# Optimization experiments

Measured on AMD Instinct MI355X. Metric: run time of the kernel, lower is better.

The kernel has to match this reference:

```python
import jax, jax.numpy as jnp
import numpy as np

SPATIAL, CROP = 128, 256


def definePsf(N, M, slope):
    # standard LCT psf (O'Toole et al.), as used in Wenzheng Chen's torch port
    x = (np.arange(2 * N, dtype=np.float32) / (2 * N - 1)) * 2 - 1
    z = (np.arange(2 * M, dtype=np.float32) / (2 * M - 1)) * 2
    gy, gx = np.meshgrid(x, x)
    psf = np.abs(((4 * slope) ** 2) * (gx[None] ** 2 + gy[None] ** 2) - z[:, None, None])
    psf = (psf == psf.min(axis=0, keepdims=True)).astype(np.float32)
    psf = psf / psf[:, N, N].sum()
    psf = psf / np.linalg.norm(psf.ravel())
    psf = np.roll(psf, N, axis=1)
    psf = np.roll(psf, N, axis=2)
    return psf


def resamplingOperator(M):
    row = M ** 2
    x = np.arange(row, dtype=np.float64) + 1
    mtx = np.zeros((row, M), dtype=np.float64)
    mtx[np.arange(row), (np.ceil(np.sqrt(x)) - 1).astype(np.int64)] = 1
    mtx = mtx / x[:, None]
    mtxi = mtx.T.copy()
    for _ in range(int(np.log2(M))):
        mtx = 0.5 * (mtx[0::2] + mtx[1::2])
        mtxi = 0.5 * (mtxi[:, 0::2] + mtxi[:, 1::2])
    return mtx.astype(np.float32), mtxi.astype(np.float32)


def setup_inputs() -> dict:
    key = jax.random.key(0)
    k1, k2 = jax.random.split(key)
    B, D, T, H = 1, 1, CROP, SPATIAL
    feture = jax.random.uniform(k1, (B, D, T, H, H), dtype=jnp.float32)

    c = 3e8
    bin_len = 0.01
    wall_size = 2.0
    trange = CROP * c * (bin_len / c)
    slope = (wall_size / 2.0) / trange
    psf = definePsf(SPATIAL, CROP, slope)
    fpsf = np.fft.fftn(psf)
    snr = 0.1
    invpsf = np.conjugate(fpsf) / (1.0 / snr + np.real(fpsf) ** 2 + np.imag(fpsf) ** 2)

    mtx, mtxi = resamplingOperator(CROP)
    gridz = (np.arange(CROP, dtype=np.float32) / (CROP - 1)).reshape(1, CROP, 1, 1)
    learnable_w = 0.01 * jax.random.normal(k2, (2,) + psf.shape, dtype=jnp.float32)

    return dict(
        feture=feture,
        gridz=jnp.asarray(gridz),
        mtx=jnp.asarray(mtx),
        mtxi=jnp.asarray(mtxi),
        invpsf_real=jnp.asarray(np.real(invpsf).astype(np.float32)),
        invpsf_imag=jnp.asarray(np.imag(invpsf).astype(np.float32)),
        learnable_w=learnable_w,
    )


def reference(feture, gridz, mtx, mtxi, invpsf_real, invpsf_imag, learnable_w):
    B, D, T, H, W = feture.shape
    # diffuse falloff compensation: * z^4
    data = feture.reshape(B * D, T, H, W) * gridz ** 4
    # temporal resampling GEMM: [M,T] @ [BD,T,HW]
    tmp = jnp.einsum('mt,bthw->bmhw', mtx, data)
    # zero-pad to 2T x 2H x 2W
    pad = jnp.zeros((B * D, 2 * T, 2 * H, 2 * W), jnp.float32).at[:, :T, :H, :W].set(tmp)
    # full (non-onesided) complex 3D FFT of real data
    fre = jnp.fft.fftn(pad, axes=(1, 2, 3))
    # learned + fixed inverse filter in frequency domain
    wf = (learnable_w[0] + invpsf_real) + 1j * (learnable_w[1] + invpsf_imag)
    vol = jnp.fft.ifftn(fre * wf, axes=(1, 2, 3)).real[:, :T, :H, :W]
    # inverse temporal resampling GEMM
    out = jnp.einsum('mt,bthw->bmhw', mtxi, vol)
    return out.reshape(B, D, T, H, W)
```

## Files before the change

### kernel.cpp

```cpp
#include <hip/hip_runtime.h>
#include <math.h>

#define TC 256
#define HC 128
#define Z2 512
#define Y2 256
#define X2 256
#define HW 16384
#define LSTR256 260
#define LSTR512 519
#define MTSH 4
#define MT (1<<MTSH)
#define WPAD 132
#define KZS 257

__device__ __forceinline__ float2 cadd(float2 a, float2 b){ return make_float2(a.x+b.x, a.y+b.y); }
__device__ __forceinline__ float2 csub(float2 a, float2 b){ return make_float2(a.x-b.x, a.y-b.y); }

template<int SGN>
__device__ __forceinline__ float2 cmul_tw(float2 z, float2 w){
  float wy = (SGN < 0) ? w.y : -w.y;
  return make_float2(z.x*w.x - z.y*wy, z.x*wy + z.y*w.x);
}
template<int SGN>
__device__ __forceinline__ float2 mul_pmi(float2 t){
  return (SGN < 0) ? make_float2(t.y, -t.x) : make_float2(-t.y, t.x);
}

template<int SGN>
__device__ __forceinline__ void dft16(float2 r[16], const float2* __restrict__ tw){
  float2 u[16];
  #pragma unroll
  for (int b2=0;b2<4;b2++){
    float2 x0=r[b2], x1=r[4+b2], x2=r[8+b2], x3=r[12+b2];
    float2 t0=cadd(x0,x2), t1=csub(x0,x2), t2=cadd(x1,x3), t3=csub(x1,x3);
    float2 y0=cadd(t0,t2), y2=csub(t0,t2);
    float2 t3i = mul_pmi<SGN>(t3);
    float2 y1=cadd(t1,t3i), y3=csub(t1,t3i);
    u[0*4+b2]=y0;
    u[1*4+b2]=cmul_tw<SGN>(y1, tw[(16*b2)&255]);
    u[2*4+b2]=cmul_tw<SGN>(y2, tw[(32*b2)&255]);
    u[3*4+b2]=cmul_tw<SGN>(y3, tw[(48*b2)&255]);
  }
  #pragma unroll
  for (int e2=0;e2<4;e2++){
    float2 x0=u[e2*4+0], x1=u[e2*4+1], x2=u[e2*4+2], x3=u[e2*4+3];
    float2 t0=cadd(x0,x2), t1=csub(x0,x2), t2=cadd(x1,x3), t3=csub(x1,x3);
    float2 t3i = mul_pmi<SGN>(t3);
    r[0*4+e2]=cadd(t0,t2);
    r[1*4+e2]=cadd(t1,t3i);
    r[2*4+e2]=csub(t0,t2);
    r[3*4+e2]=csub(t1,t3i);
  }
}

template<int SGN>
__device__ __forceinline__ void fft256(float2* ln, int b, const float2* __restrict__ tw){
  float2 r[16];
  #pragma unroll
  for (int a=0;a<16;a++) r[a] = ln[16*a+b];
  dft16<SGN>(r, tw);
  #pragma unroll
  for (int e=1;e<16;e++) r[e] = cmul_tw<SGN>(r[e], tw[(b*e)&255]);
  __syncthreads();
  #pragma unroll
  for (int e=0;e<16;e++) ln[16*e+b] = r[e];
  __syncthreads();
  #pragma unroll
  for (int a=0;a<16;a++) r[a] = ln[16*b+a];
  dft16<SGN>(r, tw);
  __syncthreads();
  #pragma unroll
  for (int d=0;d<16;d++) ln[16*d+b] = r[d];
  __syncthreads();
}

template<int SGN, bool CROP_OUT>
__device__ __forceinline__ void fft512(float2* ln, int lt,
        const float2* __restrict__ tw256, const float2* __restrict__ tw512){
  int team = lt >> 4, b = lt & 15;
  float2* sc = ln + team*256;
  float2 r[16];
  #pragma unroll
  for (int a=0;a<16;a++) r[a] = ln[2*(16*a+b) + team];
  dft16<SGN>(r, tw256);
  #pragma unroll
  for (int e=1;e<16;e++) r[e] = cmul_tw<SGN>(r[e], tw256[(b*e)&255]);
  __syncthreads();
  #pragma unroll
  for (int e=0;e<16;e++) sc[16*e+b] = r[e];
  __syncthreads();
  #pragma unroll
  for (int a=0;a<16;a++) r[a] = sc[16*b+a];
  dft16<SGN>(r, tw256);
  __syncthreads();
  if (team==0){
    #pragma unroll
    for (int d=0;d<16;d++) ln[16*d+b] = r[d];
  } else {
    #pragma unroll
    for (int d=0;d<16;d++){ int k=16*d+b; ln[256+k] = cmul_tw<SGN>(r[d], tw512[k]); }
  }
  __syncthreads();
  float2 res[8], res2[8];
  #pragma unroll
  for (int j=0;j<8;j++){
    int k = lt + 32*j;
    float2 E = ln[k], WO = ln[256+k];
    res[j]  = cadd(E,WO);
    res2[j] = csub(E,WO);
  }
  __syncthreads();
  #pragma unroll
  for (int j=0;j<8;j++){
    int k = lt + 32*j;
    ln[k] = res[j];
    if (!CROP_OUT) ln[256+k] = res2[j];
  }
  __syncthreads();
}

__global__ void k_init_tw(float2* tw256, float2* tw512){
  int j = threadIdx.x;
  if (j < 512){
    double a = -6.283185307179586476925286766559 * (double)j / 512.0;
    tw512[j] = make_float2((float)cos(a), (float)sin(a));
  }
  if (j < 256){
    double a = -6.283185307179586476925286766559 * (double)j / 256.0;
    tw256[j] = make_float2((float)cos(a), (float)sin(a));
  }
}

__global__ __launch_bounds__(256) void k_gemm(const float* __restrict__ A,
    const float* __restrict__ Bv, const float* __restrict__ gz, float* __restrict__ C){
  __shared__ float As[64][MT];
  __shared__ float zz[256];
  int tid = threadIdx.x;
  int hw0 = blockIdx.x*512 + tid*2;
  int m0 = blockIdx.y*MT;
  float2 acc[MT];
  #pragma unroll
  for (int i=0;i<MT;i++) acc[i]=make_float2(0.f,0.f);
  {
    float s = 1.f;
    if (gz){ float g = gz[tid]; float g2=g*g; s = g2*g2; }
    zz[tid] = s;
  }
  for (int t0=0;t0<256;t0+=64){
    __syncthreads();
    #pragma unroll
    for (int e=0;e<(64*MT)/256;e++){
      int idx = e*256 + tid;
      int tt = idx >> MTSH, mi = idx & (MT-1);
      As[tt][mi] = A[(size_t)(m0+mi)*256 + t0 + tt] * zz[t0+tt];
    }
    __syncthreads();
    for (int ts=0;ts<64;ts+=8){
      float2 v[8];
      #pragma unroll
      for (int j=0;j<8;j++) v[j] = *(const float2*)(Bv + (size_t)(t0+ts+j)*HW + hw0);
      #pragma unroll
      for (int j=0;j<8;j++){
        const float4* row = (const float4*)&As[ts+j][0];
        #pragma unroll
        for (int q=0;q<MT/4;q++){
          float4 a4 = row[q];
          acc[4*q+0].x += a4.x*v[j].x; acc[4*q+0].y += a4.x*v[j].y;
          acc[4*q+1].x += a4.y*v[j].x; acc[4*q+1].y += a4.y*v[j].y;
          acc[4*q+2].x += a4.z*v[j].x; acc[4*q+2].y += a4.z*v[j].y;
          acc[4*q+3].x += a4.w*v[j].x; acc[4*q+3].y += a4.w*v[j].y;
        }
      }
    }
  }
  #pragma unroll
  for (int mi=0;mi<MT;mi++) *(float2*)(C + (size_t)(m0+mi)*HW + hw0) = acc[mi];
}

__global__ __launch_bounds__(256) void k_fft_zf(const float* __restrict__ tmp,
      float2* __restrict__ A, const float2* __restrict__ tw256, const float2* __restrict__ tw512){
  __shared__ float2 buf[8*LSTR512];
  int tid = threadIdx.x;
  int w = tid & 7, lt = tid >> 3;
  int hw = blockIdx.x*8 + w;
  int h = hw >> 7, wx = hw & 127;
  float2* ln = buf + w*LSTR512;
  #pragma unroll
  for (int a=0;a<16;a++){
    int n = 32*a + lt;
    ln[n] = (n<256) ? make_float2(tmp[(size_t)n*HW + hw], 0.f) : make_float2(0.f,0.f);
  }
  __syncthreads();
  fft512<-1,false>(ln, lt, tw256, tw512);
  size_t colbase = (size_t)h*WPAD + wx;
  #pragma unroll
  for (int a=0;a<8;a++){
    int n = 32*a + lt;
    A[(size_t)n*(128*WPAD) + colbase] = ln[n];
  }
  if (lt==0) A[(size_t)256*(128*WPAD) + colbase] = ln[256];
}

__global__ __launch_bounds__(256) void k_fft_yf(const float2* __restrict__ A,
      float2* __restrict__ B, const float2* __restrict__ tw256){
  __shared__ float2 buf[16*LSTR256];
  int tid = threadIdx.x;
  int w = tid & 15, b = tid >> 4;
  int kz = blockIdx.x;
  int wx = blockIdx.y*16 + w;
  float2* ln = buf + w*LSTR256;
  size_t abase = (size_t)kz*(128*WPAD) + wx;
  #pragma unroll
  for (int a=0;a<8;a++){
    int n = 16*a + b;
    ln[n] = A[abase + (size_t)n*WPAD];
    ln[n+128] = make_float2(0.f,0.f);
  }
  __syncthreads();
  fft256<-1>(ln, b, tw256);
  size_t bbase = (size_t)kz*(256*WPAD) + wx;
  #pragma unroll
  for (int a=0;a<16;a++){
    int n = 16*a + b;
    B[bbase + (size_t)n*WPAD] = ln[n];
  }
}

__global__ __launch_bounds__(256) void k_x_filt(float2* __restrict__ B,
      const float* __restrict__ R, const float* __restrict__ I,
      const float* __restrict__ w0, const float* __restrict__ w1,
      const float2* __restrict__ tw256){
  __shared__ float2 buf[16*LSTR256];
  const float sc = 1.f/33554432.f;
  int tid = threadIdx.x;
  int wl = tid >> 4, b = tid & 15;
  int kz = blockIdx.y;
  int ky = blockIdx.x*16 + wl;
  float2* ln = buf + wl*LSTR256;
  size_t rb = ((size_t)kz*256 + ky)*WPAD;
  #pragma unroll
  for (int a=0;a<8;a++){
    int n = 16*a + b;
    ln[n] = B[rb + n];
    ln[n+128] = make_float2(0.f,0.f);
  }
  __syncthreads();
  fft256<-1>(ln, b, tw256);
  unsigned mz = (512u - (unsigned)kz) & 511u;
  unsigned my = (256u - (unsigned)ky) & 255u;
  size_t trow = ((size_t)kz<<16) + (size_t)ky*256;
  size_t mrow = ((size_t)mz<<16) + (size_t)my*256;
  #pragma unroll
  for (int a=0;a<16;a++){
    int kx = 16*a + b;
    int mx = (256 - kx) & 255;
    float wr = (R[trow+kx] + 0.5f*(w0[trow+kx] + w0[mrow+mx]))*sc;
    float wi = (I[trow+kx] + 0.5f*(w1[trow+kx] - w1[mrow+mx]))*sc;
    float2 v = ln[kx];
    ln[kx] = make_float2(v.x*wr - v.y*wi, v.x*wi + v.y*wr);
  }
  fft256<1>(ln, b, tw256);
  #pragma unroll
  for (int a=0;a<8;a++){
    int n = 16*a + b;
    B[rb + n] = ln[n];
  }
}

__global__ __launch_bounds__(256) void k_fft_yi(const float2* __restrict__ B,
      float2* __restrict__ A, const float2* __restrict__ tw256){
  __shared__ float2 buf[16*LSTR256];
  int tid = threadIdx.x;
  int w = tid & 15, b = tid >> 4;
  int kz = blockIdx.x;
  int wx = blockIdx.y*16 + w;
  float2* ln = buf + w*LSTR256;
  size_t bbase = (size_t)kz*(256*WPAD) + wx;
  #pragma unroll
  for (int a=0;a<16;a++){
    int n = 16*a + b;
    ln[n] = B[bbase + (size_t)n*WPAD];
  }
  __syncthreads();
  fft256<1>(ln, b, tw256);
  size_t abase = (size_t)kz*(128*WPAD) + wx;
  #pragma unroll
  for (int a=0;a<8;a++){
    int n = 16*a + b;
    A[abase + (size_t)n*WPAD] = ln[n];
  }
}

__global__ __launch_bounds__(256) void k_fft_zi(const float2* __restrict__ A,
      float* __restrict__ vol, const float2* __restrict__ tw256, const float2* __restrict__ tw512){
  __shared__ float2 buf[8*LSTR512];
  int tid = threadIdx.x;
  int w = tid & 7, lt = tid >> 3;
  int hw = blockIdx.x*8 + w;
  int h = hw >> 7, wx = hw & 127;
  float2* ln = buf + w*LSTR512;
  size_t colbase = (size_t)h*WPAD + wx;
  #pragma unroll
  for (int a=0;a<8;a++){
    int n = 32*a + lt;
    ln[n] = A[(size_t)n*(128*WPAD) + colbase];
  }
  if (lt==0) ln[256] = A[(size_t)256*(128*WPAD) + colbase];
  __syncthreads();
  #pragma unroll
  for (int a=8;a<16;a++){
    int n = 32*a + lt;
    if (n > 256){ float2 v = ln[512-n]; ln[n] = make_float2(v.x, -v.y); }
  }
  __syncthreads();
  fft512<1,true>(ln, lt, tw256, tw512);
  #pragma unroll
  for (int a=0;a<8;a++){
    int n = 32*a + lt;
    vol[(size_t)n*HW + hw] = ln[n].x;
  }
}

extern "C" void kernel_launch(void* const* d_in, const int* in_sizes, int n_in,
                              void* d_out, int out_size, void* d_ws, size_t ws_size,
                              hipStream_t stream) {
  const float* fet = (const float*)d_in[0];
  const float* gz  = (const float*)d_in[1];
  const float* mtx = (const float*)d_in[2];
  const float* mtxi= (const float*)d_in[3];
  const float* Rr  = (const float*)d_in[4];
  const float* Ii  = (const float*)d_in[5];
  const float* lw  = (const float*)d_in[6];
  const float* w0  = lw;
  const float* w1  = lw + (size_t)Z2*Y2*X2;
  float* out = (float*)d_out;

  char* ws = (char*)d_ws;
  const size_t OFF_TW256 = 0;
  const size_t OFF_TW512 = 2048;
  const size_t OFF_TMP   = 8192;
  const size_t TMP_BYTES = (size_t)TC*HW*sizeof(float);
  const size_t OFF_A     = OFF_TMP + TMP_BYTES;
  const size_t A_BYTES   = (size_t)KZS*128*WPAD*sizeof(float2);
  const size_t OFF_B     = OFF_A + A_BYTES;
  const size_t B_BYTES   = (size_t)KZS*256*WPAD*sizeof(float2);
  const size_t NEED      = OFF_B + B_BYTES;
  if (ws_size < NEED) return;

  float2* tw256 = (float2*)(ws + OFF_TW256);
  float2* tw512 = (float2*)(ws + OFF_TW512);
  float*  tmp   = (float*)(ws + OFF_TMP);
  float*  vol   = (float*)(ws + OFF_TMP);
  float2* A     = (float2*)(ws + OFF_A);
  float2* B     = (float2*)(ws + OFF_B);

  hipLaunchKernelGGL(k_init_tw, dim3(1), dim3(512), 0, stream, tw256, tw512);
  hipLaunchKernelGGL(k_gemm, dim3(32,256/MT), dim3(256), 0, stream, mtx, fet, gz, tmp);
  hipLaunchKernelGGL(k_fft_zf, dim3(2048), dim3(256), 0, stream, tmp, A, tw256, tw512);
  hipLaunchKernelGGL(k_fft_yf, dim3(KZS,8), dim3(256), 0, stream, A, B, tw256);
  hipLaunchKernelGGL(k_x_filt, dim3(16,KZS), dim3(256), 0, stream, B, Rr, Ii, w0, w1, tw256);
  hipLaunchKernelGGL(k_fft_yi, dim3(KZS,8), dim3(256), 0, stream, B, A, tw256);
  hipLaunchKernelGGL(k_fft_zi, dim3(2048), dim3(256), 0, stream, A, vol, tw256, tw512);
  hipLaunchKernelGGL(k_gemm, dim3(32,256/MT), dim3(256), 0, stream, mtxi, vol, (const float*)nullptr, out);
}
```

Baseline: 308.3 us.

## Fuse y-forward, x-filter and y-inverse FFTs into one per-plane kernel

After: 421.2 us. 1.37x slower.

```diff
diff --git a/kernel.cpp b/kernel.cpp
--- a/kernel.cpp
+++ b/kernel.cpp
@@ -202,93 +202,105 @@
   if (lt==0) A[(size_t)256*(128*WPAD) + colbase] = ln[256];
 }
 
-__global__ __launch_bounds__(256) void k_fft_yf(const float2* __restrict__ A,
-      float2* __restrict__ B, const float2* __restrict__ tw256){
-  __shared__ float2 buf[16*LSTR256];
-  int tid = threadIdx.x;
-  int w = tid & 15, b = tid >> 4;
-  int kz = blockIdx.x;
-  int wx = blockIdx.y*16 + w;
-  float2* ln = buf + w*LSTR256;
-  size_t abase = (size_t)kz*(128*WPAD) + wx;
-  #pragma unroll
-  for (int a=0;a<8;a++){
-    int n = 16*a + b;
-    ln[n] = A[abase + (size_t)n*WPAD];
-    ln[n+128] = make_float2(0.f,0.f);
-  }
-  __syncthreads();
-  fft256<-1>(ln, b, tw256);
-  size_t bbase = (size_t)kz*(256*WPAD) + wx;
-  #pragma unroll
-  for (int a=0;a<16;a++){
-    int n = 16*a + b;
-    B[bbase + (size_t)n*WPAD] = ln[n];
-  }
-}
-
-__global__ __launch_bounds__(256) void k_x_filt(float2* __restrict__ B,
+__global__ __launch_bounds__(512) void k_plane(float2* __restrict__ A,
       const float* __restrict__ R, const float* __restrict__ I,
       const float* __restrict__ w0, const float* __restrict__ w1,
       const float2* __restrict__ tw256){
-  __shared__ float2 buf[16*LSTR256];
+  __shared__ float2 lds[32*LSTR256];
   const float sc = 1.f/33554432.f;
   int tid = threadIdx.x;
-  int wl = tid >> 4, b = tid & 15;
-  int kz = blockIdx.y;
-  int ky = blockIdx.x*16 + wl;
-  float2* ln = buf + wl*LSTR256;
-  size_t rb = ((size_t)kz*256 + ky)*WPAD;
-  #pragma unroll
-  for (int a=0;a<8;a++){
-    int n = 16*a + b;
-    ln[n] = B[rb + n];
-    ln[n+128] = make_float2(0.f,0.f);
-  }
-  __syncthreads();
-  fft256<-1>(ln, b, tw256);
-  unsigned mz = (512u - (unsigned)kz) & 511u;
-  unsigned my = (256u - (unsigned)ky) & 255u;
-  size_t trow = ((size_t)kz<<16) + (size_t)ky*256;
-  size_t mrow = ((size_t)mz<<16) + (size_t)my*256;
-  #pragma unroll
-  for (int a=0;a<16;a++){
-    int kx = 16*a + b;
-    int mx = (256 - kx) & 255;
-    float wr = (R[trow+kx] + 0.5f*(w0[trow+kx] + w0[mrow+mx]))*sc;
-    float wi = (I[trow+kx] + 0.5f*(w1[trow+kx] - w1[mrow+mx]))*sc;
-    float2 v = ln[kx];
-    ln[kx] = make_float2(v.x*wr - v.y*wi, v.x*wi + v.y*wr);
-  }
-  fft256<1>(ln, b, tw256);
-  #pragma unroll
-  for (int a=0;a<8;a++){
-    int n = 16*a + b;
-    B[rb + n] = ln[n];
-  }
-}
-
-__global__ __launch_bounds__(256) void k_fft_yi(const float2* __restrict__ B,
-      float2* __restrict__ A, const float2* __restrict__ tw256){
-  __shared__ float2 buf[16*LSTR256];
-  int tid = threadIdx.x;
-  int w = tid & 15, b = tid >> 4;
   int kz = blockIdx.x;
-  int wx = blockIdx.y*16 + w;
-  float2* ln = buf + w*LSTR256;
-  size_t bbase = (size_t)kz*(256*WPAD) + wx;
-  #pragma unroll
-  for (int a=0;a<16;a++){
-    int n = 16*a + b;
-    ln[n] = B[bbase + (size_t)n*WPAD];
-  }
-  __syncthreads();
-  fft256<1>(ln, b, tw256);
-  size_t abase = (size_t)kz*(128*WPAD) + wx;
-  #pragma unroll
-  for (int a=0;a<8;a++){
-    int n = 16*a + b;
-    A[abase + (size_t)n*WPAD] = ln[n];
+  float2* Ap = A + (size_t)kz*(128*WPAD);
+  int r = tid >> 4, b = tid & 15;
+  int lh = tid >> 2, lc8 = (tid & 3)*8;
+  float2 pr[8][8];
+
+  #pragma unroll
+  for (int W=0; W<4; ++W){
+    {
+      const float4* src = (const float4*)(Ap + (size_t)lh*WPAD + W*32 + lc8);
+      float4 v0=src[0], v1=src[1], v2=src[2], v3=src[3];
+      lds[(lc8+0)*LSTR256 + lh] = make_float2(v0.x,v0.y);
+      lds[(lc8+1)*LSTR256 + lh] = make_float2(v0.z,v0.w);
+      lds[(lc8+2)*LSTR256 + lh] = make_float2(v1.x,v1.y);
+      lds[(lc8+3)*LSTR256 + lh] = make_float2(v1.z,v1.w);
+      lds[(lc8+4)*LSTR256 + lh] = make_float2(v2.x,v2.y);
+      lds[(lc8+5)*LSTR256 + lh] = make_float2(v2.z,v2.w);
+      lds[(lc8+6)*LSTR256 + lh] = make_float2(v3.x,v3.y);
+      lds[(lc8+7)*LSTR256 + lh] = make_float2(v3.z,v3.w);
+    }
+    {
+      int p0 = 128 + b*8;
+      #pragma unroll
+      for (int j=0;j<8;j++) lds[r*LSTR256 + p0 + j] = make_float2(0.f,0.f);
+    }
+    __syncthreads();
+    fft256<-1>(lds + r*LSTR256, b, tw256);
+    #pragma unroll
+    for (int kq=0;kq<8;kq++){
+      pr[kq][2*W]   = lds[(size_t)b*LSTR256 + kq*32 + r];
+      pr[kq][2*W+1] = lds[(size_t)(b+16)*LSTR256 + kq*32 + r];
+    }
+    __syncthreads();
+  }
+
+  #pragma unroll
+  for (int kq=0;kq<8;kq++){
+    float2* ln = lds + r*LSTR256;
+    #pragma unroll
+    for (int j=0;j<8;j++){
+      ln[b + 16*j] = pr[kq][j];
+      ln[128 + b + 16*j] = make_float2(0.f,0.f);
+    }
+    __syncthreads();
+    fft256<-1>(ln, b, tw256);
+    {
+      int ky = kq*32 + r;
+      unsigned mz = (512u - (unsigned)kz) & 511u;
+      unsigned my = (256u - (unsigned)ky) & 255u;
+      size_t trow = ((size_t)kz<<16) + (size_t)ky*256;
+      size_t mrow = ((size_t)mz<<16) + (size_t)my*256;
+      #pragma unroll
+      for (int a=0;a<16;a++){
+        int kx = 16*a + b;
+        int mx = (256 - kx) & 255;
+        float wr = (R[trow+kx] + 0.5f*(w0[trow+kx] + w0[mrow+mx]))*sc;
+        float wi = (I[trow+kx] + 0.5f*(w1[trow+kx] - w1[mrow+mx]))*sc;
+        float2 v = ln[kx];
+        ln[kx] = make_float2(v.x*wr - v.y*wi, v.x*wi + v.y*wr);
+      }
+    }
+    fft256<1>(ln, b, tw256);
+    #pragma unroll
+    for (int a=0;a<8;a++) pr[kq][a] = ln[16*a + b];
+    __syncthreads();
+  }
+
+  #pragma unroll
+  for (int W=0; W<4; ++W){
+    #pragma unroll
+    for (int kq=0;kq<8;kq++){
+      lds[(size_t)b*LSTR256 + kq*32 + r]      = pr[kq][2*W];
+      lds[(size_t)(b+16)*LSTR256 + kq*32 + r] = pr[kq][2*W+1];
+    }
+    __syncthreads();
+    fft256<1>(lds + r*LSTR256, b, tw256);
+    {
+      float2 t0 = lds[(lc8+0)*LSTR256 + lh];
+      float2 t1 = lds[(lc8+1)*LSTR256 + lh];
+      float2 t2 = lds[(lc8+2)*LSTR256 + lh];
+      float2 t3 = lds[(lc8+3)*LSTR256 + lh];
+      float2 t4 = lds[(lc8+4)*LSTR256 + lh];
+      float2 t5 = lds[(lc8+5)*LSTR256 + lh];
+      float2 t6 = lds[(lc8+6)*LSTR256 + lh];
+      float2 t7 = lds[(lc8+7)*LSTR256 + lh];
+      float4* dst = (float4*)(Ap + (size_t)lh*WPAD + W*32 + lc8);
+      dst[0] = make_float4(t0.x,t0.y,t1.x,t1.y);
+      dst[1] = make_float4(t2.x,t2.y,t3.x,t3.y);
+      dst[2] = make_float4(t4.x,t4.y,t5.x,t5.y);
+      dst[3] = make_float4(t6.x,t6.y,t7.x,t7.y);
+    }
+    __syncthreads();
   }
 }
 
@@ -343,9 +355,7 @@
   const size_t TMP_BYTES = (size_t)TC*HW*sizeof(float);
   const size_t OFF_A     = OFF_TMP + TMP_BYTES;
   const size_t A_BYTES   = (size_t)KZS*128*WPAD*sizeof(float2);
-  const size_t OFF_B     = OFF_A + A_BYTES;
-  const size_t B_BYTES   = (size_t)KZS*256*WPAD*sizeof(float2);
-  const size_t NEED      = OFF_B + B_BYTES;
+  const size_t NEED      = OFF_A + A_BYTES;
   if (ws_size < NEED) return;
 
   float2* tw256 = (float2*)(ws + OFF_TW256);
@@ -353,14 +363,11 @@
   float*  tmp   = (float*)(ws + OFF_TMP);
   float*  vol   = (float*)(ws + OFF_TMP);
   float2* A     = (float2*)(ws + OFF_A);
-  float2* B     = (float2*)(ws + OFF_B);
 
   hipLaunchKernelGGL(k_init_tw, dim3(1), dim3(512), 0, stream, tw256, tw512);
   hipLaunchKernelGGL(k_gemm, dim3(32,256/MT), dim3(256), 0, stream, mtx, fet, gz, tmp);
   hipLaunchKernelGGL(k_fft_zf, dim3(2048), dim3(256), 0, stream, tmp, A, tw256, tw512);
-  hipLaunchKernelGGL(k_fft_yf, dim3(KZS,8), dim3(256), 0, stream, A, B, tw256);
-  hipLaunchKernelGGL(k_x_filt, dim3(16,KZS), dim3(256), 0, stream, B, Rr, Ii, w0, w1, tw256);
-  hipLaunchKernelGGL(k_fft_yi, dim3(KZS,8), dim3(256), 0, stream, B, A, tw256);
+  hipLaunchKernelGGL(k_plane, dim3(KZS), dim3(512), 0, stream, A, Rr, Ii, w0, w1, tw256);
   hipLaunchKernelGGL(k_fft_zi, dim3(2048), dim3(256), 0, stream, A, vol, tw256, tw512);
   hipLaunchKernelGGL(k_gemm, dim3(32,256/MT), dim3(256), 0, stream, mtxi, vol, (const float*)nullptr, out);
 }
```
